# Performance work log

Measured on AMD Instinct MI355X. Metric: run time of the kernel, lower is better.

Reference implementation:

```python
import jax, jax.numpy as jnp
import numpy as np

ALPHA = 100.0  # self.softmax_alpha


def _interp_nearest(x, size):
    # torch F.interpolate mode='nearest': src_idx = floor(dst_idx * H_in / H_out)
    H, W = x.shape[-2], x.shape[-1]
    h, w = size
    ri = (jnp.arange(h) * H) // h
    ci = (jnp.arange(w) * W) // w
    return x[:, :, ri, :][:, :, :, ci]


def _interp_bilinear_ac(x, size):
    # torch F.interpolate mode='bilinear', align_corners=True
    H, W = x.shape[-2], x.shape[-1]
    h, w = size

    def coords(n_out, n_in):
        if n_out == 1:
            return jnp.zeros((1,), jnp.float32)
        return jnp.arange(n_out, dtype=jnp.float32) * ((n_in - 1) / (n_out - 1))

    ry, rx = coords(h, H), coords(w, W)
    y0 = jnp.floor(ry).astype(jnp.int32)
    x0 = jnp.floor(rx).astype(jnp.int32)
    y1 = jnp.clip(y0 + 1, 0, H - 1)
    x1 = jnp.clip(x0 + 1, 0, W - 1)
    wy = (ry - y0.astype(jnp.float32))[None, None, :, None]
    wx = (rx - x0.astype(jnp.float32))[None, None, None, :]
    rows = x[:, :, y0, :] * (1.0 - wy) + x[:, :, y1, :] * wy  # (n,c,h,W)
    return rows[:, :, :, x0] * (1.0 - wx) + rows[:, :, :, x1] * wx  # (n,c,h,w)


def _warp(unalign_fb, fa, fa_parse, fb, fb_parse, alpha):
    n, c, h, w = fa.shape
    c2 = unalign_fb.shape[1]
    hw = h * w
    # center and channel-normalize features per spatial location
    fa = fa - jnp.mean(fa, axis=(2, 3), keepdims=True)
    fb = fb - jnp.mean(fb, axis=(2, 3), keepdims=True)
    fa = fa.reshape(n, c, hw)
    fb = fb.reshape(n, c, hw)
    fa = fa / jnp.linalg.norm(fa, axis=1, keepdims=True)
    fb = fb / jnp.linalg.norm(fb, axis=1, keepdims=True)
    ufb = unalign_fb.reshape(n, c2, hw)
    mask_a = (fa_parse.reshape(n, -1, hw)[:, 1:, :] != 0).astype(fa.dtype)  # (n,K,hw)
    mask_b = (fb_parse.reshape(n, -1, hw)[:, 1:, :] != 0).astype(fb.dtype)
    local_fa = fa[:, None, :, :] * mask_a[:, :, None, :]  # (n,K,c,hw)
    local_fb = fb[:, None, :, :] * mask_b[:, :, None, :]  # (n,K,c,hw)
    # energy[n,k,q,p] = sum_c local_fb[n,k,c,q] * local_fa[n,k,c,p]
    energy = jnp.einsum('nkcq,nkcp->nkqp', local_fb, local_fa) * alpha
    corr = jax.nn.softmax(energy, axis=2)  # softmax over fb locations q
    warped = jnp.einsum('ncq,nkqp->nkcp', ufb, corr)  # (n,K,c2,hw)
    combined = (warped * mask_a[:, :, None, :]).sum(axis=1)  # (n,c2,hw)
    norm = jnp.maximum(mask_a.sum(axis=1, keepdims=True), 1.0)  # (n,1,hw)
    aligned = combined / norm
    return aligned.reshape(n, c2, h, w)


def setup_inputs() -> dict:
    key = jax.random.key(0)
    k1, k2, k3, k4, k5 = jax.random.split(key, 5)
    return {
        'unalign_fb': jax.random.normal(k1, (1, 64, 256, 256), jnp.float32),
        'fa': jax.random.normal(k2, (1, 256, 64, 64), jnp.float32),
        'fa_parse': jax.random.randint(k3, (1, 4, 256, 256), 0, 2).astype(jnp.int32),
        'fb': jax.random.normal(k4, (1, 256, 64, 64), jnp.float32),
        'fb_parse': jax.random.randint(k5, (1, 4, 256, 256), 0, 2).astype(jnp.int32),
    }


def reference(unalign_fb, fa, fa_parse, fb, fb_parse):
    raw_hw = unalign_fb.shape[-2:]
    feat_hw = fa.shape[-2:]
    fa_p = _interp_nearest(fa_parse, feat_hw)
    fb_p = _interp_nearest(fb_parse, feat_hw)
    ufb = _interp_bilinear_ac(unalign_fb, fb.shape[-2:])
    aligned = _warp(ufb, fa, fa_p, fb, fb_p, ALPHA)
    return _interp_bilinear_ac(aligned, raw_hw)
```

## Files before the change

### kernel.cpp

```cpp
#include <hip/hip_runtime.h>
#include <math.h>

#define HW 4096
#define CC 256
#define C2 64
#define E50f 1.928749848e-22f

typedef unsigned short USH;
typedef __attribute__((ext_vector_type(8))) _Float16 f16x8;
typedef __attribute__((ext_vector_type(8))) short bf8;
typedef __attribute__((ext_vector_type(4))) float f32x4;

__device__ __forceinline__ USH f2bf(float x) {
    unsigned u = __float_as_uint(x);
    u += 0x7fff + ((u >> 16) & 1);
    return (USH)(u >> 16);
}
__device__ __forceinline__ USH f2h(float x) {
    _Float16 h = (_Float16)x;
    return *(USH*)&h;
}

__device__ __forceinline__ void gl2lds16(const USH* g, USH* l) {
    __builtin_amdgcn_global_load_lds(
        (const __attribute__((address_space(1))) void*)g,
        (__attribute__((address_space(3))) void*)l, 16, 0, 0);
}

__global__ void k_prep1(const float* __restrict__ fa, const float* __restrict__ fb,
                        float* __restrict__ mu,
                        const float* __restrict__ ufb_src, const int* __restrict__ fb_parse,
                        USH* __restrict__ vtT, float* __restrict__ bgp) {
    __shared__ float4 sred[256];
    int t = threadIdx.x;
    if (blockIdx.x < 512) {
        int b = blockIdx.x;
        const float* src = (b < CC) ? (fa + b * HW) : (fb + (b - CC) * HW);
        float s = 0.f;
        for (int q = t; q < HW; q += 256) s += src[q];
        sred[t].x = s;
        __syncthreads();
        for (int st = 128; st > 0; st >>= 1) {
            if (t < st) sred[t].x += sred[t + st].x;
            __syncthreads();
        }
        if (t == 0) mu[b] = sred[0].x * (1.0f / HW);
        return;
    }
    int bid = blockIdx.x - 512;
    int pblk = bid & 15, c = bid >> 4;
    int p = pblk * 256 + t;
    int j = p >> 6, i = p & 63;
    int off = (4 * j) * 256 + 4 * i;
    float m0 = (fb_parse[1 * 65536 + off] != 0) ? 1.f : 0.f;
    float m1 = (fb_parse[2 * 65536 + off] != 0) ? 1.f : 0.f;
    float m2 = (fb_parse[3 * 65536 + off] != 0) ? 1.f : 0.f;
    float ry = j * (255.0f / 63.0f);
    int y0 = (int)ry; y0 = min(y0, 255); int y1 = min(y0 + 1, 255);
    float wy = ry - (float)y0;
    float rx = i * (255.0f / 63.0f);
    int x0 = (int)rx; x0 = min(x0, 255); int x1 = min(x0 + 1, 255);
    float wx = rx - (float)x0;
    const float* sc = ufb_src + c * 65536;
    float r0 = sc[y0 * 256 + x0] * (1.f - wx) + sc[y0 * 256 + x1] * wx;
    float r1 = sc[y1 * 256 + x0] * (1.f - wx) + sc[y1 * 256 + x1] * wx;
    float v = r0 * (1.f - wy) + r1 * wy;
    size_t cbase = (size_t)(p >> 5) * 8192 + (p & 31);
    vtT[cbase + (0 * 65 + c) * 32] = f2bf(v * m0);
    vtT[cbase + (1 * 65 + c) * 32] = f2bf(v * m1);
    vtT[cbase + (2 * 65 + c) * 32] = f2bf(v * m2);
    if (c == 0) {
        vtT[cbase + 64 * 32]  = f2bf(m0);
        vtT[cbase + 129 * 32] = f2bf(m1);
        vtT[cbase + 194 * 32] = f2bf(m2);
        for (int m = 195; m < 256; ++m) vtT[cbase + m * 32] = 0;
    }
    sred[t] = make_float4(v, v * m0, v * m1, v * m2);
    __syncthreads();
    for (int st = 128; st > 0; st >>= 1) {
        if (t < st) {
            float4 o = sred[t + st];
            sred[t].x += o.x; sred[t].y += o.y; sred[t].z += o.z; sred[t].w += o.w;
        }
        __syncthreads();
    }
    if (t == 0) {
        float4 r = sred[0];
        bgp[pblk * 320 + 256 + c]     = r.x;
        bgp[pblk * 320 + 0 * 65 + c]  = r.y;
        bgp[pblk * 320 + 1 * 65 + c]  = r.z;
        bgp[pblk * 320 + 2 * 65 + c]  = r.w;
    }
    __syncthreads();
    if (c == 0) {
        sred[t] = make_float4(m0, m1, m2, 0.f);
        __syncthreads();
        for (int st = 128; st > 0; st >>= 1) {
            if (t < st) {
                float4 o = sred[t + st];
                sred[t].x += o.x; sred[t].y += o.y; sred[t].z += o.z;
            }
            __syncthreads();
        }
        if (t == 0) {
            float4 r = sred[0];
            bgp[pblk * 320 + 64]  = r.x;
            bgp[pblk * 320 + 129] = r.y;
            bgp[pblk * 320 + 194] = r.z;
        }
    }
}

__global__ void k_norm_ss(const float* __restrict__ fa, const float* __restrict__ fb,
                          const float* __restrict__ mu, float* __restrict__ ssq_part) {
    int which = blockIdx.z;
    const float* src = which ? fb : fa;
    int p = blockIdx.x * 256 + threadIdx.x;
    int c0 = blockIdx.y * 32;
    float ss = 0.f;
    for (int c = c0; c < c0 + 32; ++c) {
        float v = src[c * HW + p] - mu[which * CC + c];
        ss += v * v;
    }
    ssq_part[(which * 8 + blockIdx.y) * HW + p] = ss;
}

__global__ __launch_bounds__(256) void k_norm_split_t(
    const float* __restrict__ fa, const float* __restrict__ fb,
    const float* __restrict__ mu, const float* __restrict__ ssq_part,
    USH* __restrict__ faT, USH* __restrict__ fbT) {
    __shared__ float tile[64][68];
    int which = blockIdx.z;
    const float* src = which ? fb : fa;
    USH* dst = which ? fbT : faT;
    int p0 = blockIdx.x * 64;
    int c0 = blockIdx.y * 64;
    int t = threadIdx.x;
    {
        int c_r = t >> 2, seg = t & 3;
        const float* s = &src[(size_t)(c0 + c_r) * HW + p0 + seg * 16];
#pragma unroll
        for (int k = 0; k < 4; ++k)
            *(float4*)&tile[c_r][seg * 16 + k * 4] = *(const float4*)&s[k * 4];
    }
    __syncthreads();
    {
        int p_r = t >> 2, seg = t & 3;
        int cl = seg * 16;
        float ss = 0.f;
#pragma unroll
        for (int z = 0; z < 8; ++z) ss += ssq_part[(which * 8 + z) * HW + p0 + p_r];
        float rinv = rsqrtf(ss);
        union { USH us[8]; uint4 v; } h0, h1;
#pragma unroll
        for (int j = 0; j < 8; ++j)
            h0.us[j] = f2h((tile[cl + j][p_r] - mu[which * CC + c0 + cl + j]) * rinv);
#pragma unroll
        for (int j = 0; j < 8; ++j)
            h1.us[j] = f2h((tile[cl + 8 + j][p_r] - mu[which * CC + c0 + cl + 8 + j]) * rinv);
        int kc = (c0 >> 5) + (seg >> 1);
        size_t base = (size_t)kc * 131072 + (size_t)(p0 + p_r) * 32 + (seg & 1) * 16;
        *(uint4*)&dst[base] = h0.v;
        *(uint4*)&dst[base + 8] = h1.v;
    }
}

__global__ __launch_bounds__(256, 2) void k_attn(
    const USH* __restrict__ faT, const USH* __restrict__ fbT,
    const USH* __restrict__ vtT, float* __restrict__ part) {
    __shared__ USH sA[2][2048];
    __shared__ USH sB[2][4096];
    __shared__ USH sV[2][8192];
    __shared__ USH sE[64 * 136];
    int t = threadIdx.x;
    int p0 = blockIdx.x * 64;
    int z = blockIdx.y;
    int w = t >> 6, lane = t & 63, lr = lane & 15, quad = lane >> 4;
    f32x4 accp[4][4] = {};

    const USH* gA = faT + (size_t)p0 * 32;

#define DMA_AB(buf, kc, q0)                                                          \
    do {                                                                             \
        gl2lds16(gA + (size_t)(kc) * 131072 + w * 512 + lane * 8, &sA[buf][w * 512]);\
        _Pragma("unroll")                                                            \
        for (int cc = 0; cc < 2; ++cc)                                               \
            gl2lds16(fbT + (size_t)(kc) * 131072 + (size_t)(q0) * 32 +               \
                         (2 * w + cc) * 512 + lane * 8,                              \
                     &sB[buf][(2 * w + cc) * 512]);                                  \
    } while (0)
#define DMA_V(buf, qc)                                                               \
    do {                                                                             \
        _Pragma("unroll")                                                            \
        for (int cc = 0; cc < 4; ++cc)                                               \
            gl2lds16(vtT + (size_t)(qc) * 8192 + (4 * w + cc) * 512 + lane * 8,      \
                     &sV[buf][(4 * w + cc) * 512]);                                  \
    } while (0)

    DMA_AB(0, 0, z * 512);
    __syncthreads();
    for (int qt = 0; qt < 4; ++qt) {
        int q0 = z * 512 + qt * 128;
        f32x4 accs[2][4] = {};
        for (int kc = 0; kc < 8; ++kc) {
            int cur = kc & 1;
            if (kc < 7) DMA_AB(cur ^ 1, kc + 1, q0);
            else        DMA_V(0, z * 16 + qt * 4);
            f16x8 a[2], b[4];
#pragma unroll
            for (int i = 0; i < 2; ++i)
                a[i] = *(const f16x8*)&sB[cur][(32 * w + 16 * i + lr) * 32 + quad * 8];
#pragma unroll
            for (int jj = 0; jj < 4; ++jj)
                b[jj] = *(const f16x8*)&sA[cur][(16 * jj + lr) * 32 + quad * 8];
#pragma unroll
            for (int i = 0; i < 2; ++i)
#pragma unroll
                for (int jj = 0; jj < 4; ++jj)
                    accs[i][jj] = __builtin_amdgcn_mfma_f32_16x16x32_f16(a[i], b[jj], accs[i][jj], 0, 0, 0);
            __syncthreads();
        }
#pragma unroll
        for (int i = 0; i < 2; ++i)
#pragma unroll
            for (int jj = 0; jj < 4; ++jj) {
                unsigned u0 = ((unsigned)f2bf(__expf(fmaf(100.f, accs[i][jj][1], -50.f))) << 16)
                            | (unsigned)f2bf(__expf(fmaf(100.f, accs[i][jj][0], -50.f)));
                unsigned u1 = ((unsigned)f2bf(__expf(fmaf(100.f, accs[i][jj][3], -50.f))) << 16)
                            | (unsigned)f2bf(__expf(fmaf(100.f, accs[i][jj][2], -50.f)));
                int addr = (16 * jj + lr) * 136 + 32 * w + 16 * i + 4 * quad;
                uint2 u; u.x = u0; u.y = u1;
                *(uint2*)&sE[addr] = u;
            }
        __syncthreads();
        for (int kc = 0; kc < 4; ++kc) {
            int cur = kc & 1;
            if (kc < 3)      DMA_V(cur ^ 1, z * 16 + qt * 4 + kc + 1);
            else if (qt < 3) DMA_AB(0, 0, q0 + 128);
            bf8 av[4], be[4];
#pragma unroll
            for (int i = 0; i < 4; ++i)
                av[i] = *(const bf8*)&sV[cur][(64 * w + 16 * i + lr) * 32 + quad * 8];
#pragma unroll
            for (int jj = 0; jj < 4; ++jj)
                be[jj] = *(const bf8*)&sE[(16 * jj + lr) * 136 + kc * 32 + quad * 8];
#pragma unroll
            for (int i = 0; i < 4; ++i)
#pragma unroll
                for (int jj = 0; jj < 4; ++jj)
                    accp[i][jj] = __builtin_amdgcn_mfma_f32_16x16x32_bf16(av[i], be[jj], accp[i][jj], 0, 0, 0);
            __syncthreads();
        }
    }
#undef DMA_AB
#undef DMA_V
    float* op = part + (size_t)z * 1048576;
#pragma unroll
    for (int i = 0; i < 4; ++i) {
        int m = 64 * w + 16 * i + quad * 4;
#pragma unroll
        for (int jj = 0; jj < 4; ++jj) {
            int pc = p0 + 16 * jj + lr;
#pragma unroll
            for (int r = 0; r < 4; ++r)
                op[(size_t)(m + r) * HW + pc] = accp[i][jj][r];
        }
    }
}

__global__ void k_combine8(const float* __restrict__ part, const float* __restrict__ bgp,
                           const int* __restrict__ fa_parse, float* __restrict__ aligned) {
    __shared__ float sums[8];
    int t = threadIdx.x;
    int c2 = blockIdx.y;
    if (t < 7) {
        int idx = (t < 3) ? (t * 65 + 64) : ((t < 6) ? (t - 3) * 65 + c2 : 256 + c2);
        float s = 0.f;
#pragma unroll
        for (int pb = 0; pb < 16; ++pb) s += bgp[pb * 320 + idx];
        sums[t] = s;
    }
    __syncthreads();
    int p = blockIdx.x * 256 + t;
    int jj = p >> 6, ii = p & 63;
    int off = (4 * jj) * 256 + 4 * ii;
    float num = 0.f, s = 0.f;
    for (int k = 0; k < 3; ++k) {
        float ma = (fa_parse[(k + 1) * 65536 + off] != 0) ? 1.f : 0.f;
        s += ma;
        float den = E50f * (4096.0f - sums[k]);
        float nu  = E50f * (sums[6] - sums[3 + k]);
        size_t rd = (size_t)(k * 65 + 64) * HW + p;
        size_t rn = (size_t)(k * 65 + c2) * HW + p;
#pragma unroll
        for (int z = 0; z < 8; ++z) {
            den += part[(size_t)z * 1048576 + rd];
            nu  += part[(size_t)z * 1048576 + rn];
        }
        num += ma * (nu / den);
    }
    aligned[c2 * HW + p] = num / fmaxf(s, 1.f);
}

__global__ void k_bilin_up(const float* __restrict__ aligned, float* __restrict__ out) {
    int idx = (blockIdx.x * 256 + threadIdx.x) * 4;
    int c2 = blockIdx.y;
    int y = idx >> 8;
    float ry = y * (63.0f / 255.0f);
    int y0 = (int)ry; y0 = min(y0, 63); int y1 = min(y0 + 1, 63);
    float wy = ry - (float)y0;
    const float* a = aligned + c2 * HW;
    float4 o;
    float* op = &o.x;
#pragma unroll
    for (int u = 0; u < 4; ++u) {
        int x = (idx & 255) + u;
        float rx = x * (63.0f / 255.0f);
        int x0 = (int)rx; x0 = min(x0, 63); int x1 = min(x0 + 1, 63);
        float wx = rx - (float)x0;
        float r0 = a[y0 * 64 + x0] * (1.f - wx) + a[y0 * 64 + x1] * wx;
        float r1 = a[y1 * 64 + x0] * (1.f - wx) + a[y1 * 64 + x1] * wx;
        op[u] = r0 * (1.f - wy) + r1 * wy;
    }
    *(float4*)&out[c2 * 65536 + idx] = o;
}

extern "C" void kernel_launch(void* const* d_in, const int* in_sizes, int n_in,
                              void* d_out, int out_size, void* d_ws, size_t ws_size,
                              hipStream_t stream) {
    const float* unalign_fb = (const float*)d_in[0];
    const float* fa         = (const float*)d_in[1];
    const int*   fa_parse   = (const int*)d_in[2];
    const float* fb         = (const float*)d_in[3];
    const int*   fb_parse   = (const int*)d_in[4];
    float* out = (float*)d_out;

    float* w = (float*)d_ws;
    float* mu       = w;
    float* ssq_part = w + 512;
    float* bgp      = w + 66048;
    float* part     = w + 71168;
    float* aligned  = w + 8459776;
    USH* faT = (USH*)(w + 8721920);
    USH* fbT = (USH*)(w + 9246208);
    USH* vtT = (USH*)(w + 9770496);

    k_prep1<<<dim3(1536), dim3(256), 0, stream>>>(fa, fb, mu, unalign_fb, fb_parse, vtT, bgp);
    k_norm_ss<<<dim3(16, 8, 2), dim3(256), 0, stream>>>(fa, fb, mu, ssq_part);
    k_norm_split_t<<<dim3(64, 4, 2), dim3(256), 0, stream>>>(fa, fb, mu, ssq_part, faT, fbT);
    k_attn<<<dim3(64, 8), dim3(256), 0, stream>>>(faT, fbT, vtT, part);
    k_combine8<<<dim3(16, 64), dim3(256), 0, stream>>>(part, bgp, fa_parse, aligned);
    k_bilin_up<<<dim3(64, 64), dim3(256), 0, stream>>>(aligned, out);
}
```

Before: 135.4 us.

## Load attention MFMA operands directly from global, dropping LDS staging buffers

```diff
diff --git a/kernel.cpp b/kernel.cpp
--- a/kernel.cpp
+++ b/kernel.cpp
@@ -19,12 +19,6 @@
 __device__ __forceinline__ USH f2h(float x) {
     _Float16 h = (_Float16)x;
     return *(USH*)&h;
-}
-
-__device__ __forceinline__ void gl2lds16(const USH* g, USH* l) {
-    __builtin_amdgcn_global_load_lds(
-        (const __attribute__((address_space(1))) void*)g,
-        (__attribute__((address_space(3))) void*)l, 16, 0, 0);
 }
 
 __global__ void k_prep1(const float* __restrict__ fa, const float* __restrict__ fb,
@@ -168,9 +162,6 @@
 __global__ __launch_bounds__(256, 2) void k_attn(
     const USH* __restrict__ faT, const USH* __restrict__ fbT,
     const USH* __restrict__ vtT, float* __restrict__ part) {
-    __shared__ USH sA[2][2048];
-    __shared__ USH sB[2][4096];
-    __shared__ USH sV[2][8192];
     __shared__ USH sE[64 * 136];
     int t = threadIdx.x;
     int p0 = blockIdx.x * 64;
@@ -178,48 +169,28 @@
     int w = t >> 6, lane = t & 63, lr = lane & 15, quad = lane >> 4;
     f32x4 accp[4][4] = {};
 
-    const USH* gA = faT + (size_t)p0 * 32;
-
-#define DMA_AB(buf, kc, q0)                                                          \
-    do {                                                                             \
-        gl2lds16(gA + (size_t)(kc) * 131072 + w * 512 + lane * 8, &sA[buf][w * 512]);\
-        _Pragma("unroll")                                                            \
-        for (int cc = 0; cc < 2; ++cc)                                               \
-            gl2lds16(fbT + (size_t)(kc) * 131072 + (size_t)(q0) * 32 +               \
-                         (2 * w + cc) * 512 + lane * 8,                              \
-                     &sB[buf][(2 * w + cc) * 512]);                                  \
-    } while (0)
-#define DMA_V(buf, qc)                                                               \
-    do {                                                                             \
-        _Pragma("unroll")                                                            \
-        for (int cc = 0; cc < 4; ++cc)                                               \
-            gl2lds16(vtT + (size_t)(qc) * 8192 + (4 * w + cc) * 512 + lane * 8,      \
-                     &sV[buf][(4 * w + cc) * 512]);                                  \
-    } while (0)
-
-    DMA_AB(0, 0, z * 512);
-    __syncthreads();
+    const USH* pA = faT + (size_t)(p0 + lr) * 32 + quad * 8;
+    const USH* pB = fbT + (size_t)(z * 512 + 32 * w + lr) * 32 + quad * 8;
+    const USH* pV = vtT + (size_t)(64 * w + lr) * 32 + quad * 8;
+
     for (int qt = 0; qt < 4; ++qt) {
-        int q0 = z * 512 + qt * 128;
         f32x4 accs[2][4] = {};
+#pragma unroll
         for (int kc = 0; kc < 8; ++kc) {
-            int cur = kc & 1;
-            if (kc < 7) DMA_AB(cur ^ 1, kc + 1, q0);
-            else        DMA_V(0, z * 16 + qt * 4);
             f16x8 a[2], b[4];
 #pragma unroll
             for (int i = 0; i < 2; ++i)
-                a[i] = *(const f16x8*)&sB[cur][(32 * w + 16 * i + lr) * 32 + quad * 8];
+                a[i] = *(const f16x8*)&pB[(size_t)kc * 131072 + qt * 4096 + i * 512];
 #pragma unroll
             for (int jj = 0; jj < 4; ++jj)
-                b[jj] = *(const f16x8*)&sA[cur][(16 * jj + lr) * 32 + quad * 8];
+                b[jj] = *(const f16x8*)&pA[(size_t)kc * 131072 + jj * 512];
 #pragma unroll
             for (int i = 0; i < 2; ++i)
 #pragma unroll
                 for (int jj = 0; jj < 4; ++jj)
                     accs[i][jj] = __builtin_amdgcn_mfma_f32_16x16x32_f16(a[i], b[jj], accs[i][jj], 0, 0, 0);
-            __syncthreads();
-        }
+        }
+        if (qt) __syncthreads();
 #pragma unroll
         for (int i = 0; i < 2; ++i)
 #pragma unroll
@@ -233,14 +204,14 @@
                 *(uint2*)&sE[addr] = u;
             }
         __syncthreads();
+#pragma unroll
         for (int kc = 0; kc < 4; ++kc) {
-            int cur = kc & 1;
-            if (kc < 3)      DMA_V(cur ^ 1, z * 16 + qt * 4 + kc + 1);
-            else if (qt < 3) DMA_AB(0, 0, q0 + 128);
-            bf8 av[4], be[4];
+            size_t vb = (size_t)(z * 16 + qt * 4 + kc) * 8192;
+            bf8 av[4] = {}, be[4];
 #pragma unroll
             for (int i = 0; i < 4; ++i)
-                av[i] = *(const bf8*)&sV[cur][(64 * w + 16 * i + lr) * 32 + quad * 8];
+                if (!(w == 3 && i > 0))
+                    av[i] = *(const bf8*)&pV[vb + i * 512];
 #pragma unroll
             for (int jj = 0; jj < 4; ++jj)
                 be[jj] = *(const bf8*)&sE[(16 * jj + lr) * 136 + kc * 32 + quad * 8];
@@ -248,12 +219,10 @@
             for (int i = 0; i < 4; ++i)
 #pragma unroll
                 for (int jj = 0; jj < 4; ++jj)
-                    accp[i][jj] = __builtin_amdgcn_mfma_f32_16x16x32_bf16(av[i], be[jj], accp[i][jj], 0, 0, 0);
-            __syncthreads();
-        }
-    }
-#undef DMA_AB
-#undef DMA_V
+                    if (!(w == 3 && i > 0))
+                        accp[i][jj] = __builtin_amdgcn_mfma_f32_16x16x32_bf16(av[i], be[jj], accp[i][jj], 0, 0, 0);
+        }
+    }
     float* op = part + (size_t)z * 1048576;
 #pragma unroll
     for (int i = 0; i < 4; ++i) {
@@ -263,7 +232,8 @@
             int pc = p0 + 16 * jj + lr;
 #pragma unroll
             for (int r = 0; r < 4; ++r)
-                op[(size_t)(m + r) * HW + pc] = accp[i][jj][r];
+                if (m + r < 195)
+                    op[(size_t)(m + r) * HW + pc] = accp[i][jj][r];
         }
     }
 }
```

Result: no change. 134.5 us (-0.7%).
